# Optimization experiments

Measured on AMD Instinct MI355X. Metric: run time of the kernel, lower is better.

Reference implementation:

```python
import jax, jax.numpy as jnp
import numpy as np
from jax import lax

H = 64            # GRU hidden size
NUM_LAYERS = 4
EPS = 1e-5        # BatchNorm eps
NEG_SLOPE = 0.1   # LeakyReLU slope


def setup_inputs() -> dict:
    key = jax.random.key(0)
    ks = jax.random.split(key, 24)
    B, T, D = 4096, 34, 180

    def u(k, shape, fan):
        s = 1.0 / np.sqrt(fan)
        return jax.random.uniform(k, shape, jnp.float32, -s, s)

    inp = {
        "poses": jax.random.normal(ks[0], (B, T, D), jnp.float32),
        # pre_conv: Conv1d(180,16,3) -> BN(16) -> Conv1d(16,8,3) -> BN(8) -> Conv1d(8,8,3)
        "conv1_w": u(ks[1], (16, D, 3), D * 3),
        "conv1_b": u(ks[2], (16,), D * 3),
        "bn1_g": jnp.ones((16,), jnp.float32),
        "bn1_b": jnp.zeros((16,), jnp.float32),
        "conv2_w": u(ks[3], (8, 16, 3), 16 * 3),
        "conv2_b": u(ks[4], (8,), 16 * 3),
        "bn2_g": jnp.ones((8,), jnp.float32),
        "bn2_b": jnp.zeros((8,), jnp.float32),
        "conv3_w": u(ks[5], (8, 8, 3), 8 * 3),
        "conv3_b": u(ks[6], (8,), 8 * 3),
        # GRU layer 0: input 8 -> hidden 64
        "gru0_w_ih": u(ks[7], (3 * H, 8), H),
        # GRU layers 1..3: input 64 -> hidden 64 (stacked)
        "gru_w_ih": u(ks[8], (NUM_LAYERS - 1, 3 * H, H), H),
        "gru_w_hh": u(ks[9], (NUM_LAYERS, 3 * H, H), H),
        "gru_b_ih": u(ks[10], (NUM_LAYERS, 3 * H), H),
        "gru_b_hh": u(ks[11], (NUM_LAYERS, 3 * H), H),
        "out_w": u(ks[12], (1, H), H),
        "out_b": u(ks[13], (1,), H),
        "out2_w": u(ks[14], (1, T - 6), T - 6),
        "out2_b": u(ks[15], (1,), T - 6),
    }
    return inp


def _conv1d(x, w, b):
    # x: [B, C_in, L], w: [C_out, C_in, K] -> [B, C_out, L-K+1]
    y = lax.conv_general_dilated(x, w, (1,), 'VALID',
                                 dimension_numbers=('NCH', 'OIH', 'NCH'))
    return y + b[None, :, None]


def _bn_train(x, g, b):
    # training-mode BatchNorm1d over (batch, length) per channel; x: [B, C, L]
    m = jnp.mean(x, axis=(0, 2), keepdims=True)
    v = jnp.mean(jnp.square(x - m), axis=(0, 2), keepdims=True)  # biased var
    return (x - m) * jax.lax.rsqrt(v + EPS) * g[None, :, None] + b[None, :, None]


def _leaky(x):
    return jnp.where(x >= 0, x, NEG_SLOPE * x)


def _gru_layer(x_tbh, w_ih, w_hh, b_ih, b_hh):
    # x_tbh: [T, B, D_in]; returns outputs [T, B, H]
    xg = jnp.einsum('tbi,gi->tbg', x_tbh, w_ih) + b_ih  # [T, B, 3H]

    def step(h, xg_t):
        hg = h @ w_hh.T + b_hh
        i_r, i_z, i_n = jnp.split(xg_t, 3, axis=-1)
        h_r, h_z, h_n = jnp.split(hg, 3, axis=-1)
        r = jax.nn.sigmoid(i_r + h_r)
        z = jax.nn.sigmoid(i_z + h_z)
        n = jnp.tanh(i_n + r * h_n)
        h_new = n - n * z + z * h  # == (1-z)*n + z*h
        return h_new, h_new

    B = x_tbh.shape[1]
    h0 = jnp.zeros((B, H), x_tbh.dtype)
    _, ys = lax.scan(step, h0, xg)
    return ys


def reference(poses, conv1_w, conv1_b, bn1_g, bn1_b, conv2_w, conv2_b,
              bn2_g, bn2_b, conv3_w, conv3_b, gru0_w_ih, gru_w_ih,
              gru_w_hh, gru_b_ih, gru_b_hh, out_w, out_b, out2_w, out2_b):
    x = jnp.transpose(poses, (0, 2, 1))          # [B, D, T]
    x = _leaky(_bn_train(_conv1d(x, conv1_w, conv1_b), bn1_g, bn1_b))
    x = _leaky(_bn_train(_conv1d(x, conv2_w, conv2_b), bn2_g, bn2_b))
    x = _conv1d(x, conv3_w, conv3_b)             # [B, 8, T-6]
    feat = jnp.transpose(x, (2, 0, 1))           # [T', B, 8] time-major

    out = _gru_layer(feat, gru0_w_ih, gru_w_hh[0], gru_b_ih[0], gru_b_hh[0])
    for i in range(1, NUM_LAYERS):
        out = _gru_layer(out, gru_w_ih[i - 1], gru_w_hh[i], gru_b_ih[i], gru_b_hh[i])

    out = jnp.transpose(out, (1, 0, 2))          # [B, T', H]
    y = jnp.einsum('bth,oh->bto', out, out_w)[..., 0] + out_b[0]  # [B, T']
    y = y @ out2_w[0] + out2_b[0]                # [B]
    return jax.nn.sigmoid(y)[:, None]            # [B, 1]
```

## Files before the change

kernel.cpp:

```cpp
#include <hip/hip_runtime.h>

typedef unsigned short u16;
typedef __attribute__((ext_vector_type(8))) short bf16x8;
typedef __attribute__((ext_vector_type(4))) short bf16x4;
typedef __attribute__((ext_vector_type(4))) float f32x4;

#define TP 28
#define NB 4096
#define L2E 1.4426950408889634f

__device__ __forceinline__ u16 f2bf(float x) {
  union { float f; unsigned u; } v; v.f = x;
  unsigned u = v.u;
  return (u16)((u + 0x7fffu + ((u >> 16) & 1u)) >> 16);
}
__device__ __forceinline__ float bf2f(u16 h) {
  union { unsigned u; float f; } v; v.u = ((unsigned)h) << 16; return v.f;
}
__device__ __forceinline__ float rcp_(float x) {
  float r;
  asm("v_rcp_f32 %0, %1" : "=v"(r) : "v"(x));
  return r;
}
__device__ __forceinline__ float exp2_(float x) {
  float r;
  asm("v_exp_f32 %0, %1" : "=v"(r) : "v"(x));
  return r;
}
__device__ __forceinline__ float sigm2(float x) { return rcp_(1.0f + exp2_(-x)); }
__device__ __forceinline__ float tanh2(float x) { return 1.0f - 2.0f * rcp_(1.0f + exp2_(x)); }
__device__ __forceinline__ float sigm(float x) { return rcp_(1.0f + __expf(-x)); }
__device__ __forceinline__ float leaky(float x) { return x >= 0.0f ? x : 0.1f * x; }
__device__ __forceinline__ f32x4 mfma16(bf16x8 a, bf16x8 b, f32x4 c) {
  return __builtin_amdgcn_mfma_f32_16x16x32_bf16(a, b, c, 0, 0, 0);
}
__device__ __forceinline__ bf16x8 pack8s(float4 a, float4 b, float s) {
  bf16x8 f;
  f[0] = (short)f2bf(a.x * s); f[1] = (short)f2bf(a.y * s);
  f[2] = (short)f2bf(a.z * s); f[3] = (short)f2bf(a.w * s);
  f[4] = (short)f2bf(b.x * s); f[5] = (short)f2bf(b.y * s);
  f[6] = (short)f2bf(b.z * s); f[7] = (short)f2bf(b.w * s);
  return f;
}
__device__ __forceinline__ bf16x8 ldfrag8s(const float* p, float s) {
  float4 u0 = *(const float4*)p;
  float4 u1 = *(const float4*)(p + 4);
  return pack8s(u0, u1, s);
}

__global__ __launch_bounds__(512, 4) void k_conv1(
    const float* __restrict__ poses, const float* __restrict__ w1,
    const float* __restrict__ b1, float* __restrict__ y1,
    float* __restrict__ p1)
{
  __shared__ __align__(16) u16 xs[4][6128];
  __shared__ __align__(16) u16 wt[16][544];
  __shared__ float sp[8][16];
  __shared__ float sq[8][16];
  const int tid = threadIdx.x;
  for (int i = tid; i < 16 * 544; i += 512) ((u16*)wt)[i] = 0;
  if (tid < 32) xs[tid >> 3][6120 + (tid & 7)] = 0;
  __syncthreads();
  for (int i = tid; i < 8640; i += 512) {
    int co = i / 540, r = i % 540, ci = r / 3, tap = r % 3;
    wt[co][tap * 180 + ci] = f2bf(w1[i]);
  }

  const int b0 = blockIdx.x * 4;
  const float4* s4 = (const float4*)(poses + (size_t)b0 * 6120);
  float4 rv0, rv1, rv2, rv3, rv4, rv5, rv6, rv7, rv8, rv9, rv10, rv11;
  rv0 = s4[tid];            rv1 = s4[512 + tid];   rv2 = s4[1024 + tid];
  rv3 = s4[1536 + tid];     rv4 = s4[2048 + tid];  rv5 = s4[2560 + tid];
  rv6 = s4[3072 + tid];     rv7 = s4[3584 + tid];  rv8 = s4[4096 + tid];
  rv9 = s4[4608 + tid];     rv10 = s4[5120 + tid];
  if (tid < 488) rv11 = s4[5632 + tid];
#define CVW(J, RV)                                                     \
  {                                                                    \
    int i = (J)*512 + tid;                                             \
    int bb_ = i / 1530, p4 = i - bb_ * 1530;                           \
    unsigned lo = (unsigned)f2bf(RV.x) | ((unsigned)f2bf(RV.y) << 16); \
    unsigned hi = (unsigned)f2bf(RV.z) | ((unsigned)f2bf(RV.w) << 16); \
    *(uint2*)&xs[bb_][p4 * 4] = make_uint2(lo, hi);                    \
  }
  CVW(0, rv0) CVW(1, rv1) CVW(2, rv2) CVW(3, rv3) CVW(4, rv4) CVW(5, rv5)
  CVW(6, rv6) CVW(7, rv7) CVW(8, rv8) CVW(9, rv9) CVW(10, rv10)
  if (tid < 488) CVW(11, rv11)
#undef CVW
  __syncthreads();

  const int lane = tid & 63;
  const int wv = tid >> 6;
  const int co = lane & 15;
  const int kgrp = lane >> 4;
  const int kg = kgrp * 8;
  const int R0 = kgrp * 4;
  const int bb = wv >> 1;
  const int b = b0 + bb;
  const int t0 = (wv & 1) * 16;
  const u16* pr = &xs[bb][(t0 + co) * 180];
  const float bias = b1[co];
  f32x4 acc = {bias, bias, bias, bias};

#pragma unroll
  for (int s = 0; s < 17; ++s) {
    bf16x4 lo = *(const bf16x4*)(pr + s * 32 + kg);
    bf16x4 hi = *(const bf16x4*)(pr + s * 32 + kg + 4);
    bf16x8 a0 = {lo[0], lo[1], lo[2], lo[3], hi[0], hi[1], hi[2], hi[3]};
    bf16x8 wf = *(const bf16x8*)&wt[co][s * 32 + kg];
    acc = mfma16(a0, wf, acc);
  }

  float s_ = 0.f, q_ = 0.f;
#pragma unroll
  for (int r = 0; r < 4; ++r) { s_ += acc[r]; q_ += acc[r] * acc[r]; }
  *(float4*)(y1 + (size_t)b * 512 + co * 32 + t0 + R0) =
      make_float4(acc[0], acc[1], acc[2], acc[3]);
  s_ += __shfl_xor(s_, 16); q_ += __shfl_xor(q_, 16);
  s_ += __shfl_xor(s_, 32); q_ += __shfl_xor(q_, 32);
  if (lane < 16) { sp[wv][co] = s_; sq[wv][co] = q_; }
  __syncthreads();
  if (tid < 32) {
    int ss = tid >> 4, c = tid & 15;
    float v = 0.f;
#pragma unroll
    for (int w2 = 0; w2 < 8; ++w2) v += ss ? sq[w2][c] : sp[w2][c];
    p1[blockIdx.x * 32 + ss * 16 + c] = v;
  }
}

__global__ __launch_bounds__(1024) void k_stats1(
    const float* __restrict__ p1, const float* __restrict__ g,
    const float* __restrict__ bb, float* __restrict__ sc)
{
  __shared__ float red[32][32];
  __shared__ float tot[32];
  const int tid = threadIdx.x;
  const int col = tid & 31, rg = tid >> 5;
  float a = 0;
  for (int r = rg; r < 1024; r += 32) a += p1[r * 32 + col];
  red[rg][col] = a;
  __syncthreads();
  if (tid < 32) {
    float t = 0;
    for (int i = 0; i < 32; ++i) t += red[i][tid];
    tot[tid] = t;
  }
  __syncthreads();
  if (tid < 16) {
    const float inv = 1.0f / 131072.0f;
    float m = tot[tid] * inv;
    float var = tot[16 + tid] * inv - m * m;
    float s = g[tid] * rsqrtf(fmaxf(var, 0.0f) + 1e-5f);
    sc[tid] = s;
    sc[16 + tid] = bb[tid] - m * s;
  }
}

__global__ __launch_bounds__(256) void k_conv2(
    const float* __restrict__ y1, const float* __restrict__ sc,
    const float* __restrict__ w2, const float* __restrict__ b2,
    float* __restrict__ y2, float* __restrict__ p2)
{
  __shared__ float a1[8][16][33];
  __shared__ float w2s[384];
  __shared__ float sp[4][8][2];
  const int tid = threadIdx.x;
  const int b0 = blockIdx.x * 8;
  for (int i = tid; i < 384; i += 256) w2s[i] = w2[i];
  for (int i = tid; i < 4096; i += 256) {
    int bb = i >> 9, c = (i >> 5) & 15, t = i & 31;
    float v = y1[(size_t)(b0 + bb) * 512 + c * 32 + t] * sc[c] + sc[16 + c];
    a1[bb][c][t] = leaky(v);
  }
  __syncthreads();
  float acc[8];
  const int bb = tid / 30, t = tid % 30;
  const bool act = tid < 240;
#pragma unroll
  for (int co = 0; co < 8; ++co) acc[co] = act ? b2[co] : 0.0f;
  if (act) {
    for (int ci = 0; ci < 16; ++ci) {
      float x0 = a1[bb][ci][t], x1 = a1[bb][ci][t + 1], x2 = a1[bb][ci][t + 2];
#pragma unroll
      for (int co = 0; co < 8; ++co) {
        const float* wp = &w2s[co * 48 + ci * 3];
        acc[co] += x0 * wp[0] + x1 * wp[1] + x2 * wp[2];
      }
    }
    for (int co = 0; co < 8; ++co)
      y2[(size_t)(b0 + bb) * 240 + co * 30 + t] = acc[co];
  }
  const int w = tid >> 6;
#pragma unroll
  for (int co = 0; co < 8; ++co) {
    float s = act ? acc[co] : 0.0f;
    float q = s * s;
#pragma unroll
    for (int m = 1; m <= 32; m <<= 1) { s += __shfl_xor(s, m); q += __shfl_xor(q, m); }
    if ((tid & 63) == 0) { sp[w][co][0] = s; sp[w][co][1] = q; }
  }
  __syncthreads();
  if (tid < 16) {
    int s = tid >> 3, c = tid & 7;
    p2[blockIdx.x * 16 + s * 8 + c] = sp[0][c][s] + sp[1][c][s] + sp[2][c][s] + sp[3][c][s];
  }
}

__global__ __launch_bounds__(256) void k_stats2(
    const float* __restrict__ p2, const float* __restrict__ g,
    const float* __restrict__ bb, float* __restrict__ sc)
{
  __shared__ float red[16][16];
  __shared__ float tot[16];
  const int tid = threadIdx.x;
  const int col = tid & 15, r0 = tid >> 4;
  float a = 0;
  for (int r = r0; r < 512; r += 16) a += p2[r * 16 + col];
  red[r0][col] = a;
  __syncthreads();
  if (tid < 16) {
    float t = 0;
    for (int i = 0; i < 16; ++i) t += red[i][tid];
    tot[tid] = t;
  }
  __syncthreads();
  if (tid < 8) {
    const float inv = 1.0f / 122880.0f;
    float m = tot[tid] * inv;
    float var = tot[8 + tid] * inv - m * m;
    float s = g[tid] * rsqrtf(fmaxf(var, 0.0f) + 1e-5f);
    sc[32 + tid] = s;
    sc[40 + tid] = bb[tid] - m * s;
  }
}

__global__ __launch_bounds__(256) void k_conv3(
    const float* __restrict__ y2, const float* __restrict__ sc,
    const float* __restrict__ w3, const float* __restrict__ b3,
    u16* __restrict__ feat)
{
  __shared__ float a2[8][8][31];
  __shared__ float w3s[192];
  const int tid = threadIdx.x;
  const int b0 = blockIdx.x * 8;
  for (int i = tid; i < 192; i += 256) w3s[i] = w3[i];
  for (int i = tid; i < 1920; i += 256) {
    int bb = i / 240, rem = i % 240, c = rem / 30, t = rem % 30;
    float v = y2[(size_t)(b0 + bb) * 240 + c * 30 + t] * sc[32 + c] + sc[40 + c];
    a2[bb][c][t] = leaky(v);
  }
  __syncthreads();
  if (tid < 224) {
    int bb = tid / 28, t = tid % 28;
    float acc[8];
#pragma unroll
    for (int co = 0; co < 8; ++co) acc[co] = b3[co];
    for (int ci = 0; ci < 8; ++ci) {
      float x0 = a2[bb][ci][t], x1 = a2[bb][ci][t + 1], x2 = a2[bb][ci][t + 2];
#pragma unroll
      for (int co = 0; co < 8; ++co) {
        const float* wp = &w3s[co * 24 + ci * 3];
        acc[co] += x0 * wp[0] + x1 * wp[1] + x2 * wp[2];
      }
    }
    union { u16 h[8]; uint4 v; } u;
#pragma unroll
    for (int co = 0; co < 8; ++co) u.h[co] = f2bf(acc[co]);
    *(uint4*)&feat[((size_t)t * NB + b0 + bb) * 8] = u.v;
  }
}

__global__ __launch_bounds__(1024) void k_gru_pipe(
    const u16* __restrict__ feat,
    const float* __restrict__ g0wih,
    const float* __restrict__ gwih,
    const float* __restrict__ gwhh,
    const float* __restrict__ gbih,
    const float* __restrict__ gbhh,
    const float* __restrict__ ow, const float* __restrict__ ob,
    const float* __restrict__ o2w, const float* __restrict__ o2b,
    float* __restrict__ out)
{
  __shared__ __align__(16) u16 xl[2][16][40];
  __shared__ __align__(16) u16 hl[4][2][16][72];
  __shared__ float sph[4][16];
  const int tid = threadIdx.x;
  const int b0 = blockIdx.x * 16;
  const int lane = tid & 63;
  const int wv = tid >> 6;
  const int l = wv >> 2;
  const int c = wv & 3;
  const int row = lane & 15;
  const int kgrp = lane >> 4;
  const int kg = kgrp * 8;
  const int R0 = kgrp * 4;
  const int cr = c * 16 + row;

  for (int i = tid; i < 4 * 2 * 16 * 72; i += 1024) ((u16*)hl)[i] = 0;
  for (int i = tid; i < 2 * 16 * 40; i += 1024) ((u16*)xl)[i] = 0;

  bf16x8 Wx[3][2], Wh[3][2];
  if (l == 0) {
#pragma unroll
    for (int g = 0; g < 3; ++g) {
      const float sc_ = (g == 2) ? 2.f * L2E : L2E;
      bf16x8 z;
#pragma unroll
      for (int j = 0; j < 8; ++j) z[j] = 0;
      if (kg == 0) z = ldfrag8s(g0wih + (g * 64 + cr) * 8, sc_);
      Wx[g][0] = z;
      Wx[g][1] = z;
    }
  } else {
#pragma unroll
    for (int g = 0; g < 3; ++g) {
      const float sc_ = (g == 2) ? 2.f * L2E : L2E;
#pragma unroll
      for (int s = 0; s < 2; ++s)
        Wx[g][s] = ldfrag8s(gwih + (l - 1) * 12288 + (g * 64 + cr) * 64 + s * 32 + kg, sc_);
    }
  }
#pragma unroll
  for (int g = 0; g < 3; ++g) {
    const float sc_ = (g == 2) ? 2.f * L2E : L2E;
#pragma unroll
    for (int s = 0; s < 2; ++s)
      Wh[g][s] = ldfrag8s(gwhh + l * 12288 + (g * 64 + cr) * 64 + s * 32 + kg, sc_);
  }

  const float br = (gbih[l * 192 + cr] + gbhh[l * 192 + cr]) * L2E;
  const float bz = (gbih[l * 192 + 64 + cr] + gbhh[l * 192 + 64 + cr]) * L2E;
  const float bi = gbih[l * 192 + 128 + cr] * 2.f * L2E;
  const float bh = gbhh[l * 192 + 128 + cr] * 2.f * L2E;

  float hold[4] = {0.f, 0.f, 0.f, 0.f};
  float accL[4] = {0.f, 0.f, 0.f, 0.f};
  const float owv = ow[cr];

  uint2 pf = make_uint2(0u, 0u);
  const bool xldr = (wv == 0 && lane < 32);
  if (xldr)
    pf = *(const uint2*)(feat + ((size_t)0 * NB + b0 + (lane >> 1)) * 8 + (lane & 1) * 4);
  __syncthreads();
  if (xldr)
    *(uint2*)&xl[0][lane >> 1][(lane & 1) * 4] = pf;
  __syncthreads();

  for (int tick = 0; tick < TP + 3; ++tick) {
    const int t = tick - l;
    if (t >= 0 && t < TP) {
      const int cur = t & 1, nxt = cur ^ 1;
      bf16x8 ax0, ax1, ah0, ah1;
      if (l == 0) {
        ax0 = *(const bf16x8*)&xl[cur][row][kg];
      } else {
        ax0 = *(const bf16x8*)&hl[l - 1][nxt][row][kg];
        ax1 = *(const bf16x8*)&hl[l - 1][nxt][row][32 + kg];
      }
      ah0 = *(const bf16x8*)&hl[l][cur][row][kg];
      ah1 = *(const bf16x8*)&hl[l][cur][row][32 + kg];
      if (xldr && t + 1 < TP)
        pf = *(const uint2*)(feat + ((size_t)(t + 1) * NB + b0 + (lane >> 1)) * 8 + (lane & 1) * 4);

      f32x4 ar = {br, br, br, br};
      f32x4 az = {bz, bz, bz, bz};
      f32x4 ai = {bi, bi, bi, bi};
      f32x4 an = {bh, bh, bh, bh};

      __builtin_amdgcn_s_setprio(1);
      ar = mfma16(ax0, Wx[0][0], ar);
      az = mfma16(ax0, Wx[1][0], az);
      ai = mfma16(ax0, Wx[2][0], ai);
      if (l != 0) {
        ar = mfma16(ax1, Wx[0][1], ar);
        az = mfma16(ax1, Wx[1][1], az);
        ai = mfma16(ax1, Wx[2][1], ai);
      }
      ar = mfma16(ah0, Wh[0][0], ar);
      ar = mfma16(ah1, Wh[0][1], ar);
      az = mfma16(ah0, Wh[1][0], az);
      az = mfma16(ah1, Wh[1][1], az);
      an = mfma16(ah0, Wh[2][0], an);
      an = mfma16(ah1, Wh[2][1], an);
      __builtin_amdgcn_s_setprio(0);

      float o2 = 0.f;
      if (l == 3) o2 = o2w[t];
      u16 hb[4];
#pragma unroll
      for (int r = 0; r < 4; ++r) {
        float rr = sigm2(ar[r]);
        float zz = sigm2(az[r]);
        float nn = tanh2(ai[r] + rr * an[r]);
        float hv = nn + zz * (hold[r] - nn);
        hold[r] = hv;
        hb[r] = f2bf(hv);
        if (l == 3) accL[r] += hv * owv * o2;
      }
#pragma unroll
      for (int r = 0; r < 4; ++r) hl[l][nxt][R0 + r][cr] = hb[r];
      if (xldr && t + 1 < TP)
        *(uint2*)&xl[nxt][lane >> 1][(lane & 1) * 4] = pf;
    }
    __syncthreads();
  }

  if (l == 3) {
#pragma unroll
    for (int r = 0; r < 4; ++r) {
      accL[r] += __shfl_xor(accL[r], 1);
      accL[r] += __shfl_xor(accL[r], 2);
      accL[r] += __shfl_xor(accL[r], 4);
      accL[r] += __shfl_xor(accL[r], 8);
    }
    if ((lane & 15) == 0) {
#pragma unroll
      for (int r = 0; r < 4; ++r) sph[c][R0 + r] = accL[r];
    }
  }
  __syncthreads();
  if (tid < 16) {
    float s = sph[0][tid] + sph[1][tid] + sph[2][tid] + sph[3][tid];
    float so2 = 0.f;
    for (int t = 0; t < TP; ++t) so2 += o2w[t];
    out[b0 + tid] = sigm(s + ob[0] * so2 + o2b[0]);
  }
}

extern "C" void kernel_launch(void* const* d_in, const int* in_sizes, int n_in,
                              void* d_out, int out_size, void* d_ws, size_t ws_size,
                              hipStream_t stream)
{
  const float* poses = (const float*)d_in[0];
  const float* c1w = (const float*)d_in[1];
  const float* c1b = (const float*)d_in[2];
  const float* bn1g = (const float*)d_in[3];
  const float* bn1b = (const float*)d_in[4];
  const float* c2w = (const float*)d_in[5];
  const float* c2b = (const float*)d_in[6];
  const float* bn2g = (const float*)d_in[7];
  const float* bn2b = (const float*)d_in[8];
  const float* c3w = (const float*)d_in[9];
  const float* c3b = (const float*)d_in[10];
  const float* g0wih = (const float*)d_in[11];
  const float* gwih = (const float*)d_in[12];
  const float* gwhh = (const float*)d_in[13];
  const float* gbih = (const float*)d_in[14];
  const float* gbhh = (const float*)d_in[15];
  const float* ow = (const float*)d_in[16];
  const float* ob = (const float*)d_in[17];
  const float* o2w = (const float*)d_in[18];
  const float* o2b = (const float*)d_in[19];

  float* ws = (float*)d_ws;
  float* y1 = ws;
  float* y2 = ws + 2097152;
  u16* feat = (u16*)(ws + 3080192);
  float* p1 = ws + 3538944;
  float* p2 = ws + 3604480;
  float* sc = ws + 3612672;
  float* outv = (float*)d_out;

  k_conv1<<<dim3(1024), dim3(512), 0, stream>>>(poses, c1w, c1b, y1, p1);
  k_stats1<<<dim3(1), dim3(1024), 0, stream>>>(p1, bn1g, bn1b, sc);
  k_conv2<<<dim3(512), dim3(256), 0, stream>>>(y1, sc, c2w, c2b, y2, p2);
  k_stats2<<<dim3(1), dim3(256), 0, stream>>>(p2, bn2g, bn2b, sc);
  k_conv3<<<dim3(512), dim3(256), 0, stream>>>(y2, sc, c3w, c3b, feat);
  k_gru_pipe<<<dim3(256), dim3(1024), 0, stream>>>(feat, g0wih, gwih, gwhh,
                                                   gbih, gbhh, ow, ob, o2w, o2b, outv);
}
```

Before: 111.3 us.

## Load conv1 input directly into LDS as fp32 via global_load_lds, smaller blocks

Measured after the change: 126.3 us. +13.5%, slower.

```diff
diff --git a/kernel.cpp b/kernel.cpp
--- a/kernel.cpp
+++ b/kernel.cpp
@@ -48,48 +48,41 @@
   return pack8s(u0, u1, s);
 }
 
-__global__ __launch_bounds__(512, 4) void k_conv1(
+__global__ __launch_bounds__(256, 2) void k_conv1(
     const float* __restrict__ poses, const float* __restrict__ w1,
     const float* __restrict__ b1, float* __restrict__ y1,
     float* __restrict__ p1)
 {
-  __shared__ __align__(16) u16 xs[4][6128];
+  __shared__ __align__(16) float xsf[12288];
   __shared__ __align__(16) u16 wt[16][544];
-  __shared__ float sp[8][16];
-  __shared__ float sq[8][16];
-  const int tid = threadIdx.x;
-  for (int i = tid; i < 16 * 544; i += 512) ((u16*)wt)[i] = 0;
-  if (tid < 32) xs[tid >> 3][6120 + (tid & 7)] = 0;
-  __syncthreads();
-  for (int i = tid; i < 8640; i += 512) {
-    int co = i / 540, r = i % 540, ci = r / 3, tap = r % 3;
-    wt[co][tap * 180 + ci] = f2bf(w1[i]);
-  }
-
-  const int b0 = blockIdx.x * 4;
-  const float4* s4 = (const float4*)(poses + (size_t)b0 * 6120);
-  float4 rv0, rv1, rv2, rv3, rv4, rv5, rv6, rv7, rv8, rv9, rv10, rv11;
-  rv0 = s4[tid];            rv1 = s4[512 + tid];   rv2 = s4[1024 + tid];
-  rv3 = s4[1536 + tid];     rv4 = s4[2048 + tid];  rv5 = s4[2560 + tid];
-  rv6 = s4[3072 + tid];     rv7 = s4[3584 + tid];  rv8 = s4[4096 + tid];
-  rv9 = s4[4608 + tid];     rv10 = s4[5120 + tid];
-  if (tid < 488) rv11 = s4[5632 + tid];
-#define CVW(J, RV)                                                     \
-  {                                                                    \
-    int i = (J)*512 + tid;                                             \
-    int bb_ = i / 1530, p4 = i - bb_ * 1530;                           \
-    unsigned lo = (unsigned)f2bf(RV.x) | ((unsigned)f2bf(RV.y) << 16); \
-    unsigned hi = (unsigned)f2bf(RV.z) | ((unsigned)f2bf(RV.w) << 16); \
-    *(uint2*)&xs[bb_][p4 * 4] = make_uint2(lo, hi);                    \
-  }
-  CVW(0, rv0) CVW(1, rv1) CVW(2, rv2) CVW(3, rv3) CVW(4, rv4) CVW(5, rv5)
-  CVW(6, rv6) CVW(7, rv7) CVW(8, rv8) CVW(9, rv9) CVW(10, rv10)
-  if (tid < 488) CVW(11, rv11)
-#undef CVW
-  __syncthreads();
-
+  __shared__ float sp[4][16];
+  __shared__ float sq[4][16];
+  const int tid = threadIdx.x;
   const int lane = tid & 63;
   const int wv = tid >> 6;
+  const int b0 = blockIdx.x * 2;
+
+  {
+    const long limit = (long)NB * 1530 - 1;
+#pragma unroll
+    for (int j = 0; j < 12; ++j) {
+      const int c = wv * 12 + j;
+      long fidx = (long)b0 * 1530 + (long)(c * 64 + lane);
+      if (fidx > limit) fidx = limit;
+      __builtin_amdgcn_global_load_lds(
+          (const __attribute__((address_space(1))) void*)(poses + fidx * 4),
+          (__attribute__((address_space(3))) void*)(xsf + c * 256),
+          16, 0, 0);
+    }
+  }
+
+  if (tid < 64) wt[tid >> 2][540 + (tid & 3)] = 0;
+  for (int i = tid; i < 8640; i += 256) {
+    int co_ = i / 540, r = i % 540, ci = r / 3, tap = r % 3;
+    wt[co_][tap * 180 + ci] = f2bf(w1[i]);
+  }
+  __syncthreads();
+
   const int co = lane & 15;
   const int kgrp = lane >> 4;
   const int kg = kgrp * 8;
@@ -97,15 +90,19 @@
   const int bb = wv >> 1;
   const int b = b0 + bb;
   const int t0 = (wv & 1) * 16;
-  const u16* pr = &xs[bb][(t0 + co) * 180];
+  const float* pr = xsf + bb * 6120 + (t0 + co) * 180;
   const float bias = b1[co];
   f32x4 acc = {bias, bias, bias, bias};
 
 #pragma unroll
   for (int s = 0; s < 17; ++s) {
-    bf16x4 lo = *(const bf16x4*)(pr + s * 32 + kg);
-    bf16x4 hi = *(const bf16x4*)(pr + s * 32 + kg + 4);
-    bf16x8 a0 = {lo[0], lo[1], lo[2], lo[3], hi[0], hi[1], hi[2], hi[3]};
+    f32x4 lo = *(const f32x4*)(pr + s * 32 + kg);
+    f32x4 hi = *(const f32x4*)(pr + s * 32 + kg + 4);
+    bf16x8 a0;
+    a0[0] = (short)f2bf(lo[0]); a0[1] = (short)f2bf(lo[1]);
+    a0[2] = (short)f2bf(lo[2]); a0[3] = (short)f2bf(lo[3]);
+    a0[4] = (short)f2bf(hi[0]); a0[5] = (short)f2bf(hi[1]);
+    a0[6] = (short)f2bf(hi[2]); a0[7] = (short)f2bf(hi[3]);
     bf16x8 wf = *(const bf16x8*)&wt[co][s * 32 + kg];
     acc = mfma16(a0, wf, acc);
   }
@@ -121,9 +118,8 @@
   __syncthreads();
   if (tid < 32) {
     int ss = tid >> 4, c = tid & 15;
-    float v = 0.f;
-#pragma unroll
-    for (int w2 = 0; w2 < 8; ++w2) v += ss ? sq[w2][c] : sp[w2][c];
+    float v = ss ? (sq[0][c] + sq[1][c] + sq[2][c] + sq[3][c])
+                 : (sp[0][c] + sp[1][c] + sp[2][c] + sp[3][c]);
     p1[blockIdx.x * 32 + ss * 16 + c] = v;
   }
 }
@@ -137,7 +133,7 @@
   const int tid = threadIdx.x;
   const int col = tid & 31, rg = tid >> 5;
   float a = 0;
-  for (int r = rg; r < 1024; r += 32) a += p1[r * 32 + col];
+  for (int r = rg; r < 2048; r += 32) a += p1[r * 32 + col];
   red[rg][col] = a;
   __syncthreads();
   if (tid < 32) {
@@ -400,7 +396,7 @@
 #pragma unroll
       for (int r = 0; r < 4; ++r) hl[l][nxt][R0 + r][cr] = hb[r];
       if (xldr && t + 1 < TP)
-        *(uint2*)&xl[nxt][lane >> 1][(lane & 1) * 4] = pf;
+        *(uint2*)&xl[(t + 1) & 1][lane >> 1][(lane & 1) * 4] = pf;
     }
     __syncthreads();
   }
@@ -461,7 +457,7 @@
   float* sc = ws + 3612672;
   float* outv = (float*)d_out;
 
-  k_conv1<<<dim3(1024), dim3(512), 0, stream>>>(poses, c1w, c1b, y1, p1);
+  k_conv1<<<dim3(2048), dim3(256), 0, stream>>>(poses, c1w, c1b, y1, p1);
   k_stats1<<<dim3(1), dim3(1024), 0, stream>>>(p1, bn1g, bn1b, sc);
   k_conv2<<<dim3(512), dim3(256), 0, stream>>>(y1, sc, c2w, c2b, y2, p2);
   k_stats2<<<dim3(1), dim3(256), 0, stream>>>(p2, bn2g, bn2b, sc);
```
